# Optimization experiments

Measured on AMD Instinct MI355X. Metric: run time of the kernel, lower is better.

The kernel has to match this reference:

```python
import jax, jax.numpy as jnp
import numpy as np

B, N_PER_G, H, K, A, GNN_STEPS = 64, 100, 64, 5, 50, 3
N = B * N_PER_G  # total nodes


def _lin(key, din, dout):
    s = 1.0 / np.sqrt(din)
    kw, kb = jax.random.split(key)
    w = jax.random.uniform(kw, (din, dout), minval=-s, maxval=s, dtype=jnp.float32)
    b = jax.random.uniform(kb, (dout,), minval=-s, maxval=s, dtype=jnp.float32)
    return w, b


def setup_inputs() -> dict:
    key = jax.random.key(0)
    ks = jax.random.split(key, 16)
    # complete graph (no self loops) per batch graph
    i, j = np.meshgrid(np.arange(N_PER_G), np.arange(N_PER_G), indexing="ij")
    m = i != j
    s0, d0 = i[m], j[m]  # [n*(n-1)]
    offs = (np.arange(B) * N_PER_G)[:, None]
    src = jnp.asarray((s0[None, :] + offs).reshape(-1), dtype=jnp.int32)
    dst = jnp.asarray((d0[None, :] + offs).reshape(-1), dtype=jnp.int32)
    E = src.shape[0]
    e_type = jax.random.uniform(ks[0], (E, 2), dtype=jnp.float32)
    d = jax.random.uniform(ks[1], (E, 1), dtype=jnp.float32)
    label = jax.nn.one_hot(jax.random.randint(ks[2], (N,), 0, K), K, dtype=jnp.float32)
    actions = jax.random.randint(ks[3], (B * A, 2), 0, N_PER_G)
    l1_w, l1_b = _lin(ks[4], K, H)
    l2_w, l2_b = _lin(ks[5], H, H)
    t3_w, t3_b = _lin(ks[6], H, H)
    t4_wf, t4_b = _lin(ks[7], 1, H)
    t5_wf, t5_b = _lin(ks[8], H, 1)
    t6_w, t6_b = _lin(ks[9], H, H)
    t7_1_w, t7_1_b = _lin(ks[10], H, H)
    t7_2_w, t7_2_b = _lin(ks[11], H, H)
    t9_1_w, t9_1_b = _lin(ks[12], H, H)
    t9_2_w, t9_2_b = _lin(ks[13], H, H)
    return dict(label=label, e_type=e_type, d=d,
                l1_w=l1_w, l1_b=l1_b, l2_w=l2_w, l2_b=l2_b,
                t3_w=t3_w, t3_b=t3_b, t4_w=t4_wf[0], t4_b=t4_b,
                t5_w=t5_wf[:, 0], t5_b=t5_b, t6_w=t6_w, t6_b=t6_b,
                t7_1_w=t7_1_w, t7_1_b=t7_1_b, t7_2_w=t7_2_w, t7_2_b=t7_2_b,
                t9_1_w=t9_1_w, t9_1_b=t9_1_b, t9_2_w=t9_2_w, t9_2_b=t9_2_b,
                src=src, dst=dst, actions=actions)


def reference(label, e_type, d, l1_w, l1_b, l2_w, l2_b, t3_w, t3_b, t4_w, t4_b,
              t5_w, t5_b, t6_w, t6_b, t7_1_w, t7_1_b, t7_2_w, t7_2_b,
              t9_1_w, t9_1_b, t9_2_w, t9_2_b, src, dst, actions):
    e1 = e_type[:, 0]
    # n1_hd = h[src]*e1, n1_d = d*e1; bmm(n1_hd^T, n1_d) == sum over in-edges of h[src]*e1^2*d
    w_e = (e1 * e1) * d[:, 0]                              # [E]
    s_e = d[:, 0] * e1                                     # per-edge n1_d scalar [E]
    # sum_deg relu(t4(n1_d)) as edge-parallel relu + scatter-add
    t4_edge = jax.nn.relu(s_e[:, None] * t4_w[None, :] + t4_b)   # [E,H]
    t4_sum = jax.ops.segment_sum(t4_edge, dst, num_segments=N)   # [N,H]
    base = label @ l1_w + l1_b + t4_sum @ t3_w + t3_b            # constant across gnn steps
    h = jnp.zeros((N, H), dtype=label.dtype)
    for _ in range(GNN_STEPS):
        n1_h = jax.ops.segment_sum(h[src] * w_e[:, None], dst, num_segments=N)  # [N,H]
        h = jax.nn.relu(base + n1_h @ l2_w + l2_b)
    # readout (forward_): graph mean -> t6 stem; per-action node-pair branch
    stem = h.reshape(B, N_PER_G, H).mean(axis=1) @ t6_w + t6_b    # [B,H]
    h2 = h @ t7_1_w + t7_1_b                                      # [N,H]
    offs = jnp.repeat(jnp.arange(B, dtype=actions.dtype) * N_PER_G, A)
    a = actions + offs[:, None]                                   # global node ids [B*A,2]
    ha = h2[a[:, 0]] + h2[a[:, 1]]                                # [B*A,H]
    u = jax.nn.relu(jax.nn.relu(ha) @ t7_2_w + t7_2_b) @ t9_2_w + t9_2_b
    g_branch = jax.nn.relu(stem) @ t9_1_w + t9_1_b                # [B,H]
    q = jax.nn.relu(g_branch[:, None, :] + u.reshape(B, A, H))    # [B,A,H]
    Q_sa = q.reshape(B * A, H) @ t5_w + t5_b[0]                   # [B*A]
    return Q_sa
```

## Files before the change

kernel.cpp:

```cpp
#include <hip/hip_runtime.h>

#define HD 64
#define NPG 100
#define NGRP 64
#define NACT 50
#define EPG 9900
#define CHR 13
#define ACH 13

typedef const float* fcp;

__global__ __launch_bounds__(256)
void k_edge_base(fcp label, fcp e_type, fcp dvec,
                 fcp l1_w, fcp l1_b, fcp l2_b,
                 fcp t3_w, fcp t3_b, fcp t4_w, fcp t4_b,
                 float* __restrict__ Wt, float* __restrict__ baseo,
                 float* __restrict__ hA)
{
    const int g   = blockIdx.x >> 3;
    const int c   = blockIdx.x & 7;
    const int j0  = c * CHR;
    const int cnt = (j0 + CHR <= NPG) ? CHR : (NPG - j0);
    const int t   = threadIdx.x;
    const int hh  = t & 63;
    const int w   = t >> 6;

    __shared__ __align__(16) float s_ld[CHR * 100];
    __shared__ __align__(16) float w_ld[CHR * 100];
    __shared__ __align__(16) float t4s[CHR * HD];

    float lab[4][5], l1r[5];
    #pragma unroll
    for (int kk = 0; kk < 5; ++kk) l1r[kk] = l1_w[kk * HD + hh];
    #pragma unroll
    for (int m = 0; m < 4; ++m) {
        const int jl = w + 4 * m;
        #pragma unroll
        for (int kk = 0; kk < 5; ++kk)
            lab[m][kk] = (jl < cnt) ? label[(g * NPG + j0 + jl) * 5 + kk] : 0.f;
    }

    const float2* et2 = (const float2*)e_type;
    const int ebase = g * EPG;
    for (int idx = t; idx < CHR * 100; idx += 256) {
        const int i  = idx / CHR;
        const int jl = idx - i * CHR;
        const int j  = j0 + jl;
        if (j < NPG) {
            float s = 0.f, wv = 0.f;
            if (i != j) {
                const int e = ebase + i * 99 + j - (j > i ? 1 : 0);
                const float e1 = et2[e].x;
                const float dd = dvec[e];
                s  = dd * e1;
                wv = e1 * e1 * dd;
            }
            s_ld[jl * 100 + i] = s;
            w_ld[jl * 100 + i] = wv;
        }
    }
    __syncthreads();

    {
        float* wd = Wt + g * (NPG * NPG) + j0 * NPG;
        for (int idx = t; idx < cnt * 100; idx += 256) wd[idx] = w_ld[idx];
    }

    const float w4  = t4_w[hh];
    const float b4  = t4_b[hh];
    const float rb4 = fmaxf(b4, 0.f);
    #pragma unroll
    for (int m = 0; m < 4; ++m) {
        const int jl = w + 4 * m;
        if (jl < cnt) {
            float a0 = 0.f, a1 = 0.f, a2 = 0.f, a3 = 0.f;
            #pragma unroll 5
            for (int ib = 0; ib < 25; ++ib) {
                const float4 s4 = *(const float4*)&s_ld[jl * 100 + 4 * ib];
                a0 += fmaxf(s4.x * w4 + b4, 0.f);
                a1 += fmaxf(s4.y * w4 + b4, 0.f);
                a2 += fmaxf(s4.z * w4 + b4, 0.f);
                a3 += fmaxf(s4.w * w4 + b4, 0.f);
            }
            t4s[jl * HD + hh] = (a0 + a1) + (a2 + a3) - rb4;
        }
    }

    const float bb   = l1_b[hh] + t3_b[hh];
    const float l2bv = l2_b[hh];
    float v[4];
    #pragma unroll
    for (int m = 0; m < 4; ++m) {
        float x = bb;
        #pragma unroll
        for (int kk = 0; kk < 5; ++kk) x += lab[m][kk] * l1r[kk];
        v[m] = x;
    }
    for (int ib = 0; ib < 16; ++ib) {
        const float tw0 = t3_w[(4 * ib + 0) * HD + hh];
        const float tw1 = t3_w[(4 * ib + 1) * HD + hh];
        const float tw2 = t3_w[(4 * ib + 2) * HD + hh];
        const float tw3 = t3_w[(4 * ib + 3) * HD + hh];
        #pragma unroll
        for (int m = 0; m < 4; ++m) {
            const int jl = w + 4 * m;
            if (jl < cnt) {
                const float4 x4 = *(const float4*)&t4s[jl * HD + 4 * ib];
                v[m] += x4.x * tw0 + x4.y * tw1 + x4.z * tw2 + x4.w * tw3;
            }
        }
    }
    #pragma unroll
    for (int m = 0; m < 4; ++m) {
        const int jl = w + 4 * m;
        if (jl < cnt) {
            const int n = g * NPG + j0 + jl;
            baseo[n * HD + hh] = v[m];
            hA[n * HD + hh]    = fmaxf(v[m] + l2bv, 0.f);
        }
    }
}

__global__ __launch_bounds__(256)
void k_gnn_step(const float* __restrict__ Wt, const float* __restrict__ baseo,
                const float* __restrict__ h_old, fcp l2_w, fcp l2_b,
                float* __restrict__ h_new)
{
    const int g   = blockIdx.x >> 3;
    const int c   = blockIdx.x & 7;
    const int j0  = c * CHR;
    const int cnt = (j0 + CHR <= NPG) ? CHR : (NPG - j0);
    const int t   = threadIdx.x;
    const int hh  = t & 63;
    const int w   = t >> 6;

    __shared__ __align__(16) float hs[NPG * HD];
    __shared__ __align__(16) float wr[CHR * 100];
    __shared__ __align__(16) float n1s[CHR * HD];

    float bs[4];
    #pragma unroll
    for (int m = 0; m < 4; ++m) {
        const int jl = w + 4 * m;
        bs[m] = (jl < cnt) ? baseo[(g * NPG + j0 + jl) * HD + hh] : 0.f;
    }

    {
        const float4* ho4 = (const float4*)(h_old + g * NPG * HD);
        float4* hs4 = (float4*)hs;
        for (int idx = t; idx < NPG * HD / 4; idx += 256) hs4[idx] = ho4[idx];
        const float* wsrc = Wt + g * (NPG * NPG) + j0 * NPG;
        for (int idx = t; idx < cnt * 100; idx += 256) wr[idx] = wsrc[idx];
    }
    __syncthreads();

    float acc[4];
    #pragma unroll
    for (int m = 0; m < 4; ++m) acc[m] = 0.f;
    for (int ib = 0; ib < 25; ++ib) {
        const float h0 = hs[(4 * ib + 0) * HD + hh];
        const float h1 = hs[(4 * ib + 1) * HD + hh];
        const float h2 = hs[(4 * ib + 2) * HD + hh];
        const float h3 = hs[(4 * ib + 3) * HD + hh];
        #pragma unroll
        for (int m = 0; m < 4; ++m) {
            const int jl = w + 4 * m;
            if (jl < cnt) {
                const float4 wv = *(const float4*)&wr[jl * 100 + 4 * ib];
                acc[m] += wv.x * h0 + wv.y * h1 + wv.z * h2 + wv.w * h3;
            }
        }
    }
    #pragma unroll
    for (int m = 0; m < 4; ++m) {
        const int jl = w + 4 * m;
        if (jl < cnt) n1s[jl * HD + hh] = acc[m];
    }

    const float l2bv = l2_b[hh];
    float v[4];
    #pragma unroll
    for (int m = 0; m < 4; ++m) v[m] = bs[m] + l2bv;
    for (int ib = 0; ib < 16; ++ib) {
        const float w0 = l2_w[(4 * ib + 0) * HD + hh];
        const float w1 = l2_w[(4 * ib + 1) * HD + hh];
        const float w2 = l2_w[(4 * ib + 2) * HD + hh];
        const float w3 = l2_w[(4 * ib + 3) * HD + hh];
        #pragma unroll
        for (int m = 0; m < 4; ++m) {
            const int jl = w + 4 * m;
            if (jl < cnt) {
                const float4 x4 = *(const float4*)&n1s[jl * HD + 4 * ib];
                v[m] += x4.x * w0 + x4.y * w1 + x4.z * w2 + x4.w * w3;
            }
        }
    }
    #pragma unroll
    for (int m = 0; m < 4; ++m) {
        const int jl = w + 4 * m;
        if (jl < cnt) h_new[(g * NPG + j0 + jl) * HD + hh] = fmaxf(v[m], 0.f);
    }
}

__global__ __launch_bounds__(256)
void k_tail(const float* __restrict__ hfin, const int* __restrict__ actions,
            fcp t5_w, fcp t5_b, fcp t6_w, fcp t6_b,
            fcp t7_1_w, fcp t7_1_b, fcp t7_2_w, fcp t7_2_b,
            fcp t9_1_w, fcp t9_1_b, fcp t9_2_w, fcp t9_2_b,
            float* __restrict__ out)
{
    const int g    = blockIdx.x >> 2;
    const int c    = blockIdx.x & 3;
    const int a0g  = c * ACH;
    const int acnt = (a0g + ACH <= NACT) ? ACH : (NACT - a0g);
    const int t    = threadIdx.x;
    const int hh   = t & 63;
    const int aw   = t >> 6;

    __shared__ __align__(16) float hsb[NPG * HD];
    __shared__ __align__(16) float hsum[ACH * HD];
    __shared__ __align__(16) float r1s[ACH * HD];
    __shared__ __align__(16) float awk[4 * HD];
    __shared__ float gbuf[HD];

    int a0r[5], a1r[5];
    #pragma unroll
    for (int m = 0; m < 5; ++m) {
        const int al = aw + 3 * m;
        a0r[m] = 0; a1r[m] = 0;
        if (aw < 3 && al < acnt) {
            const int a = g * NACT + a0g + al;
            a0r[m] = actions[a * 2 + 0];
            a1r[m] = actions[a * 2 + 1];
        }
    }

    {
        const float4* hg4 = (const float4*)(hfin + g * NPG * HD);
        float4* hs4 = (float4*)hsb;
        for (int idx = t; idx < NPG * HD / 4; idx += 256) hs4[idx] = hg4[idx];
    }
    __syncthreads();

    {
        float m = 0.f;
        for (int j = aw; j < NPG; j += 4) m += hsb[j * HD + hh];
        awk[aw * HD + hh] = m;
    }
    #pragma unroll
    for (int m = 0; m < 5; ++m) {
        const int al = aw + 3 * m;
        if (aw < 3 && al < acnt)
            hsum[al * HD + hh] = hsb[a0r[m] * HD + hh] + hsb[a1r[m] * HD + hh];
    }
    __syncthreads();

    if (aw == 3) {
        float ml = (awk[0 * HD + hh] + awk[1 * HD + hh])
                 + (awk[2 * HD + hh] + awk[3 * HD + hh]);
        ml *= (1.f / NPG);
        float s = t6_b[hh];
        #pragma unroll 8
        for (int q = 0; q < HD; ++q) s += __shfl(ml, q, 64) * t6_w[q * HD + hh];
        s = fmaxf(s, 0.f);
        float gb = t9_1_b[hh];
        #pragma unroll 8
        for (int q = 0; q < HD; ++q) gb += __shfl(s, q, 64) * t9_1_w[q * HD + hh];
        gbuf[hh] = gb;
    } else {
        const float b71 = 2.f * t7_1_b[hh];
        float r[5];
        #pragma unroll
        for (int m = 0; m < 5; ++m) r[m] = b71;
        for (int ib = 0; ib < 16; ++ib) {
            const float w0 = t7_1_w[(4 * ib + 0) * HD + hh];
            const float w1 = t7_1_w[(4 * ib + 1) * HD + hh];
            const float w2 = t7_1_w[(4 * ib + 2) * HD + hh];
            const float w3 = t7_1_w[(4 * ib + 3) * HD + hh];
            #pragma unroll
            for (int m = 0; m < 5; ++m) {
                const int al = aw + 3 * m;
                if (al < acnt) {
                    const float4 x4 = *(const float4*)&hsum[al * HD + 4 * ib];
                    r[m] += x4.x * w0 + x4.y * w1 + x4.z * w2 + x4.w * w3;
                }
            }
        }
        #pragma unroll
        for (int m = 0; m < 5; ++m) {
            const int al = aw + 3 * m;
            if (al < acnt) r1s[al * HD + hh] = fmaxf(r[m], 0.f);
        }
        const float b72 = t7_2_b[hh];
        #pragma unroll
        for (int m = 0; m < 5; ++m) r[m] = b72;
        for (int ib = 0; ib < 16; ++ib) {
            const float w0 = t7_2_w[(4 * ib + 0) * HD + hh];
            const float w1 = t7_2_w[(4 * ib + 1) * HD + hh];
            const float w2 = t7_2_w[(4 * ib + 2) * HD + hh];
            const float w3 = t7_2_w[(4 * ib + 3) * HD + hh];
            #pragma unroll
            for (int m = 0; m < 5; ++m) {
                const int al = aw + 3 * m;
                if (al < acnt) {
                    const float4 x4 = *(const float4*)&r1s[al * HD + 4 * ib];
                    r[m] += x4.x * w0 + x4.y * w1 + x4.z * w2 + x4.w * w3;
                }
            }
        }
        #pragma unroll
        for (int m = 0; m < 5; ++m) {
            const int al = aw + 3 * m;
            if (al < acnt) hsum[al * HD + hh] = fmaxf(r[m], 0.f);
        }
    }
    __syncthreads();

    if (aw < 3) {
        const float b92  = t9_2_b[hh];
        const float t5wv = t5_w[hh];
        const float t5bv = t5_b[0];
        const float gbv  = gbuf[hh];
        float u[5];
        #pragma unroll
        for (int m = 0; m < 5; ++m) u[m] = b92;
        for (int ib = 0; ib < 16; ++ib) {
            const float w0 = t9_2_w[(4 * ib + 0) * HD + hh];
            const float w1 = t9_2_w[(4 * ib + 1) * HD + hh];
            const float w2 = t9_2_w[(4 * ib + 2) * HD + hh];
            const float w3 = t9_2_w[(4 * ib + 3) * HD + hh];
            #pragma unroll
            for (int m = 0; m < 5; ++m) {
                const int al = aw + 3 * m;
                if (al < acnt) {
                    const float4 x4 = *(const float4*)&hsum[al * HD + 4 * ib];
                    u[m] += x4.x * w0 + x4.y * w1 + x4.z * w2 + x4.w * w3;
                }
            }
        }
        #pragma unroll
        for (int m = 0; m < 5; ++m) {
            const int al = aw + 3 * m;
            float qv = fmaxf(gbv + u[m], 0.f) * t5wv;
            #pragma unroll
            for (int off = 32; off > 0; off >>= 1) qv += __shfl_xor(qv, off, 64);
            if (al < acnt && hh == 0) out[g * NACT + a0g + al] = qv + t5bv;
        }
    }
}

extern "C" void kernel_launch(void* const* d_in, const int* in_sizes, int n_in,
                              void* d_out, int out_size, void* d_ws, size_t ws_size,
                              hipStream_t stream)
{
    fcp label  = (fcp)d_in[0];
    fcp e_type = (fcp)d_in[1];
    fcp dvec   = (fcp)d_in[2];
    fcp l1_w   = (fcp)d_in[3];
    fcp l1_b   = (fcp)d_in[4];
    fcp l2_w   = (fcp)d_in[5];
    fcp l2_b   = (fcp)d_in[6];
    fcp t3_w   = (fcp)d_in[7];
    fcp t3_b   = (fcp)d_in[8];
    fcp t4_w   = (fcp)d_in[9];
    fcp t4_b   = (fcp)d_in[10];
    fcp t5_w   = (fcp)d_in[11];
    fcp t5_b   = (fcp)d_in[12];
    fcp t6_w   = (fcp)d_in[13];
    fcp t6_b   = (fcp)d_in[14];
    fcp t7_1_w = (fcp)d_in[15];
    fcp t7_1_b = (fcp)d_in[16];
    fcp t7_2_w = (fcp)d_in[17];
    fcp t7_2_b = (fcp)d_in[18];
    fcp t9_1_w = (fcp)d_in[19];
    fcp t9_1_b = (fcp)d_in[20];
    fcp t9_2_w = (fcp)d_in[21];
    fcp t9_2_b = (fcp)d_in[22];
    const int* actions = (const int*)d_in[25];

    char* ws = (char*)d_ws;
    float* Wt   = (float*)(ws);
    float* base = (float*)(ws + 2560000);
    float* hA   = (float*)(ws + 2560000 + 1638400);
    float* hB   = (float*)(ws + 2560000 + 2 * 1638400);

    k_edge_base<<<dim3(NGRP * 8), dim3(256), 0, stream>>>(
        label, e_type, dvec, l1_w, l1_b, l2_b, t3_w, t3_b, t4_w, t4_b,
        Wt, base, hA);
    k_gnn_step<<<dim3(NGRP * 8), dim3(256), 0, stream>>>(Wt, base, hA, l2_w, l2_b, hB);
    k_gnn_step<<<dim3(NGRP * 8), dim3(256), 0, stream>>>(Wt, base, hB, l2_w, l2_b, hA);
    k_tail<<<dim3(NGRP * 4), dim3(256), 0, stream>>>(
        hA, actions, t5_w, t5_b, t6_w, t6_b, t7_1_w, t7_1_b, t7_2_w, t7_2_b,
        t9_1_w, t9_1_b, t9_2_w, t9_2_b, (float*)d_out);
}
```

Before: 182.8 us.

## Fuse edge, GNN steps and readout into one cooperative persistent kernel

Merges the four kernels into a single cooperative launch of 256 blocks, each handling 25 target nodes of one graph, with grid.sync between GNN steps. The per-block edge weight tile and the base activations now stay in shared memory and registers, so Wt and base are no longer written to and read back from global memory. Launch overhead and inter-kernel gaps go away, at the cost of grid-wide barriers, fewer blocks (lower parallelism), h now read straight from global/L2 instead of being staged in shared memory, and more registers per thread.

```diff
diff --git a/kernel.cpp b/kernel.cpp
--- a/kernel.cpp
+++ b/kernel.cpp
@@ -1,52 +1,50 @@
 #include <hip/hip_runtime.h>
+#include <hip/hip_cooperative_groups.h>
+
+namespace cg = cooperative_groups;
 
 #define HD 64
 #define NPG 100
 #define NGRP 64
 #define NACT 50
 #define EPG 9900
-#define CHR 13
-#define ACH 13
 
 typedef const float* fcp;
 
 __global__ __launch_bounds__(256)
-void k_edge_base(fcp label, fcp e_type, fcp dvec,
-                 fcp l1_w, fcp l1_b, fcp l2_b,
-                 fcp t3_w, fcp t3_b, fcp t4_w, fcp t4_b,
-                 float* __restrict__ Wt, float* __restrict__ baseo,
-                 float* __restrict__ hA)
+void k_coop(fcp label, fcp e_type, fcp dvec,
+            fcp l1_w, fcp l1_b, fcp l2_w, fcp l2_b,
+            fcp t3_w, fcp t3_b, fcp t4_w, fcp t4_b,
+            fcp t5_w, fcp t5_b, fcp t6_w, fcp t6_b,
+            fcp t7_1_w, fcp t7_1_b, fcp t7_2_w, fcp t7_2_b,
+            fcp t9_1_w, fcp t9_1_b, fcp t9_2_w, fcp t9_2_b,
+            const int* __restrict__ actions,
+            float* __restrict__ hA, float* __restrict__ hB,
+            float* __restrict__ out)
 {
-    const int g   = blockIdx.x >> 3;
-    const int c   = blockIdx.x & 7;
-    const int j0  = c * CHR;
-    const int cnt = (j0 + CHR <= NPG) ? CHR : (NPG - j0);
-    const int t   = threadIdx.x;
-    const int hh  = t & 63;
-    const int w   = t >> 6;
-
-    __shared__ __align__(16) float s_ld[CHR * 100];
-    __shared__ __align__(16) float w_ld[CHR * 100];
-    __shared__ __align__(16) float t4s[CHR * HD];
-
-    float lab[4][5], l1r[5];
-    #pragma unroll
-    for (int kk = 0; kk < 5; ++kk) l1r[kk] = l1_w[kk * HD + hh];
-    #pragma unroll
-    for (int m = 0; m < 4; ++m) {
-        const int jl = w + 4 * m;
-        #pragma unroll
-        for (int kk = 0; kk < 5; ++kk)
-            lab[m][kk] = (jl < cnt) ? label[(g * NPG + j0 + jl) * 5 + kk] : 0.f;
-    }
-
-    const float2* et2 = (const float2*)e_type;
-    const int ebase = g * EPG;
-    for (int idx = t; idx < CHR * 100; idx += 256) {
-        const int i  = idx / CHR;
-        const int jl = idx - i * CHR;
-        const int j  = j0 + jl;
-        if (j < NPG) {
+    cg::grid_group grid = cg::this_grid();
+    const int g  = blockIdx.x >> 2;
+    const int c  = blockIdx.x & 3;
+    const int j0 = c * 25;
+    const int t  = threadIdx.x;
+    const int hh = t & 63;
+    const int w  = t >> 6;
+
+    __shared__ __align__(16) float wtc[2500];
+    __shared__ __align__(16) float buf[6400];
+    __shared__ __align__(16) float awk[4 * HD];
+    __shared__ float gbuf[HD];
+
+    float* s_ld = buf;
+    float* aux  = buf + 2500;
+
+    {
+        const float2* et2 = (const float2*)e_type;
+        const int ebase = g * EPG;
+        for (int idx = t; idx < 2500; idx += 256) {
+            const int i  = idx / 25;
+            const int jl = idx - i * 25;
+            const int j  = j0 + jl;
             float s = 0.f, wv = 0.f;
             if (i != j) {
                 const int e = ebase + i * 99 + j - (j > i ? 1 : 0);
@@ -56,23 +54,18 @@
                 wv = e1 * e1 * dd;
             }
             s_ld[jl * 100 + i] = s;
-            w_ld[jl * 100 + i] = wv;
+            wtc[jl * 100 + i] = wv;
         }
     }
     __syncthreads();
-
-    {
-        float* wd = Wt + g * (NPG * NPG) + j0 * NPG;
-        for (int idx = t; idx < cnt * 100; idx += 256) wd[idx] = w_ld[idx];
-    }
 
     const float w4  = t4_w[hh];
     const float b4  = t4_b[hh];
     const float rb4 = fmaxf(b4, 0.f);
     #pragma unroll
-    for (int m = 0; m < 4; ++m) {
+    for (int m = 0; m < 7; ++m) {
         const int jl = w + 4 * m;
-        if (jl < cnt) {
+        if (jl < 25) {
             float a0 = 0.f, a1 = 0.f, a2 = 0.f, a3 = 0.f;
             #pragma unroll 5
             for (int ib = 0; ib < 25; ++ib) {
@@ -82,180 +75,140 @@
                 a2 += fmaxf(s4.z * w4 + b4, 0.f);
                 a3 += fmaxf(s4.w * w4 + b4, 0.f);
             }
-            t4s[jl * HD + hh] = (a0 + a1) + (a2 + a3) - rb4;
-        }
-    }
-
-    const float bb   = l1_b[hh] + t3_b[hh];
+            aux[jl * HD + hh] = (a0 + a1) + (a2 + a3) - rb4;
+        }
+    }
+
+    float base_r[7];
+    {
+        float l1r[5];
+        #pragma unroll
+        for (int kk = 0; kk < 5; ++kk) l1r[kk] = l1_w[kk * HD + hh];
+        const float bb = l1_b[hh] + t3_b[hh];
+        #pragma unroll
+        for (int m = 0; m < 7; ++m) {
+            const int jl = w + 4 * m;
+            float x = bb;
+            if (jl < 25) {
+                const float* lr = &label[(g * NPG + j0 + jl) * 5];
+                #pragma unroll
+                for (int kk = 0; kk < 5; ++kk) x += lr[kk] * l1r[kk];
+            }
+            base_r[m] = x;
+        }
+        for (int ib = 0; ib < 16; ++ib) {
+            const float tw0 = t3_w[(4 * ib + 0) * HD + hh];
+            const float tw1 = t3_w[(4 * ib + 1) * HD + hh];
+            const float tw2 = t3_w[(4 * ib + 2) * HD + hh];
+            const float tw3 = t3_w[(4 * ib + 3) * HD + hh];
+            #pragma unroll
+            for (int m = 0; m < 7; ++m) {
+                const int jl = w + 4 * m;
+                if (jl < 25) {
+                    const float4 x4 = *(const float4*)&aux[jl * HD + 4 * ib];
+                    base_r[m] += x4.x * tw0 + x4.y * tw1 + x4.z * tw2 + x4.w * tw3;
+                }
+            }
+        }
+    }
     const float l2bv = l2_b[hh];
-    float v[4];
     #pragma unroll
-    for (int m = 0; m < 4; ++m) {
-        float x = bb;
-        #pragma unroll
-        for (int kk = 0; kk < 5; ++kk) x += lab[m][kk] * l1r[kk];
-        v[m] = x;
-    }
-    for (int ib = 0; ib < 16; ++ib) {
-        const float tw0 = t3_w[(4 * ib + 0) * HD + hh];
-        const float tw1 = t3_w[(4 * ib + 1) * HD + hh];
-        const float tw2 = t3_w[(4 * ib + 2) * HD + hh];
-        const float tw3 = t3_w[(4 * ib + 3) * HD + hh];
-        #pragma unroll
-        for (int m = 0; m < 4; ++m) {
+    for (int m = 0; m < 7; ++m) {
+        const int jl = w + 4 * m;
+        if (jl < 25) hA[(g * NPG + j0 + jl) * HD + hh] = fmaxf(base_r[m] + l2bv, 0.f);
+    }
+    grid.sync();
+
+    const float* hsrc = hA;
+    float*       hdst = hB;
+    for (int step = 0; step < 2; ++step) {
+        const float* hgp = hsrc + g * NPG * HD + hh;
+        float acc[7];
+        #pragma unroll
+        for (int m = 0; m < 7; ++m) acc[m] = 0.f;
+        for (int ib = 0; ib < 25; ++ib) {
+            const float h0 = hgp[(4 * ib + 0) * HD];
+            const float h1 = hgp[(4 * ib + 1) * HD];
+            const float h2 = hgp[(4 * ib + 2) * HD];
+            const float h3 = hgp[(4 * ib + 3) * HD];
+            #pragma unroll
+            for (int m = 0; m < 7; ++m) {
+                const int jl = w + 4 * m;
+                if (jl < 25) {
+                    const float4 wv = *(const float4*)&wtc[jl * 100 + 4 * ib];
+                    acc[m] += wv.x * h0 + wv.y * h1 + wv.z * h2 + wv.w * h3;
+                }
+            }
+        }
+        #pragma unroll
+        for (int m = 0; m < 7; ++m) {
             const int jl = w + 4 * m;
-            if (jl < cnt) {
-                const float4 x4 = *(const float4*)&t4s[jl * HD + 4 * ib];
-                v[m] += x4.x * tw0 + x4.y * tw1 + x4.z * tw2 + x4.w * tw3;
-            }
-        }
-    }
-    #pragma unroll
-    for (int m = 0; m < 4; ++m) {
-        const int jl = w + 4 * m;
-        if (jl < cnt) {
-            const int n = g * NPG + j0 + jl;
-            baseo[n * HD + hh] = v[m];
-            hA[n * HD + hh]    = fmaxf(v[m] + l2bv, 0.f);
-        }
-    }
-}
-
-__global__ __launch_bounds__(256)
-void k_gnn_step(const float* __restrict__ Wt, const float* __restrict__ baseo,
-                const float* __restrict__ h_old, fcp l2_w, fcp l2_b,
-                float* __restrict__ h_new)
-{
-    const int g   = blockIdx.x >> 3;
-    const int c   = blockIdx.x & 7;
-    const int j0  = c * CHR;
-    const int cnt = (j0 + CHR <= NPG) ? CHR : (NPG - j0);
-    const int t   = threadIdx.x;
-    const int hh  = t & 63;
-    const int w   = t >> 6;
-
-    __shared__ __align__(16) float hs[NPG * HD];
-    __shared__ __align__(16) float wr[CHR * 100];
-    __shared__ __align__(16) float n1s[CHR * HD];
-
-    float bs[4];
-    #pragma unroll
-    for (int m = 0; m < 4; ++m) {
-        const int jl = w + 4 * m;
-        bs[m] = (jl < cnt) ? baseo[(g * NPG + j0 + jl) * HD + hh] : 0.f;
-    }
-
-    {
-        const float4* ho4 = (const float4*)(h_old + g * NPG * HD);
-        float4* hs4 = (float4*)hs;
-        for (int idx = t; idx < NPG * HD / 4; idx += 256) hs4[idx] = ho4[idx];
-        const float* wsrc = Wt + g * (NPG * NPG) + j0 * NPG;
-        for (int idx = t; idx < cnt * 100; idx += 256) wr[idx] = wsrc[idx];
-    }
-    __syncthreads();
-
-    float acc[4];
-    #pragma unroll
-    for (int m = 0; m < 4; ++m) acc[m] = 0.f;
-    for (int ib = 0; ib < 25; ++ib) {
-        const float h0 = hs[(4 * ib + 0) * HD + hh];
-        const float h1 = hs[(4 * ib + 1) * HD + hh];
-        const float h2 = hs[(4 * ib + 2) * HD + hh];
-        const float h3 = hs[(4 * ib + 3) * HD + hh];
-        #pragma unroll
-        for (int m = 0; m < 4; ++m) {
+            if (jl < 25) aux[jl * HD + hh] = acc[m];
+        }
+        float v[7];
+        #pragma unroll
+        for (int m = 0; m < 7; ++m) v[m] = base_r[m] + l2bv;
+        for (int ib = 0; ib < 16; ++ib) {
+            const float w0 = l2_w[(4 * ib + 0) * HD + hh];
+            const float w1 = l2_w[(4 * ib + 1) * HD + hh];
+            const float w2 = l2_w[(4 * ib + 2) * HD + hh];
+            const float w3 = l2_w[(4 * ib + 3) * HD + hh];
+            #pragma unroll
+            for (int m = 0; m < 7; ++m) {
+                const int jl = w + 4 * m;
+                if (jl < 25) {
+                    const float4 x4 = *(const float4*)&aux[jl * HD + 4 * ib];
+                    v[m] += x4.x * w0 + x4.y * w1 + x4.z * w2 + x4.w * w3;
+                }
+            }
+        }
+        #pragma unroll
+        for (int m = 0; m < 7; ++m) {
             const int jl = w + 4 * m;
-            if (jl < cnt) {
-                const float4 wv = *(const float4*)&wr[jl * 100 + 4 * ib];
-                acc[m] += wv.x * h0 + wv.y * h1 + wv.z * h2 + wv.w * h3;
-            }
-        }
-    }
-    #pragma unroll
-    for (int m = 0; m < 4; ++m) {
-        const int jl = w + 4 * m;
-        if (jl < cnt) n1s[jl * HD + hh] = acc[m];
-    }
-
-    const float l2bv = l2_b[hh];
-    float v[4];
-    #pragma unroll
-    for (int m = 0; m < 4; ++m) v[m] = bs[m] + l2bv;
-    for (int ib = 0; ib < 16; ++ib) {
-        const float w0 = l2_w[(4 * ib + 0) * HD + hh];
-        const float w1 = l2_w[(4 * ib + 1) * HD + hh];
-        const float w2 = l2_w[(4 * ib + 2) * HD + hh];
-        const float w3 = l2_w[(4 * ib + 3) * HD + hh];
-        #pragma unroll
-        for (int m = 0; m < 4; ++m) {
-            const int jl = w + 4 * m;
-            if (jl < cnt) {
-                const float4 x4 = *(const float4*)&n1s[jl * HD + 4 * ib];
-                v[m] += x4.x * w0 + x4.y * w1 + x4.z * w2 + x4.w * w3;
-            }
-        }
-    }
-    #pragma unroll
-    for (int m = 0; m < 4; ++m) {
-        const int jl = w + 4 * m;
-        if (jl < cnt) h_new[(g * NPG + j0 + jl) * HD + hh] = fmaxf(v[m], 0.f);
-    }
-}
-
-__global__ __launch_bounds__(256)
-void k_tail(const float* __restrict__ hfin, const int* __restrict__ actions,
-            fcp t5_w, fcp t5_b, fcp t6_w, fcp t6_b,
-            fcp t7_1_w, fcp t7_1_b, fcp t7_2_w, fcp t7_2_b,
-            fcp t9_1_w, fcp t9_1_b, fcp t9_2_w, fcp t9_2_b,
-            float* __restrict__ out)
-{
-    const int g    = blockIdx.x >> 2;
-    const int c    = blockIdx.x & 3;
-    const int a0g  = c * ACH;
-    const int acnt = (a0g + ACH <= NACT) ? ACH : (NACT - a0g);
-    const int t    = threadIdx.x;
-    const int hh   = t & 63;
-    const int aw   = t >> 6;
-
-    __shared__ __align__(16) float hsb[NPG * HD];
-    __shared__ __align__(16) float hsum[ACH * HD];
-    __shared__ __align__(16) float r1s[ACH * HD];
-    __shared__ __align__(16) float awk[4 * HD];
-    __shared__ float gbuf[HD];
+            if (jl < 25) hdst[(g * NPG + j0 + jl) * HD + hh] = fmaxf(v[m], 0.f);
+        }
+        grid.sync();
+        const float* tmp = hsrc; hsrc = hdst; hdst = (float*)tmp;
+    }
+
+    const int a0g  = c * 13;
+    const int acnt = (c < 3) ? 13 : 11;
 
     int a0r[5], a1r[5];
     #pragma unroll
     for (int m = 0; m < 5; ++m) {
-        const int al = aw + 3 * m;
+        const int al = w + 3 * m;
         a0r[m] = 0; a1r[m] = 0;
-        if (aw < 3 && al < acnt) {
+        if (w < 3 && al < acnt) {
             const int a = g * NACT + a0g + al;
             a0r[m] = actions[a * 2 + 0];
             a1r[m] = actions[a * 2 + 1];
         }
     }
-
     {
-        const float4* hg4 = (const float4*)(hfin + g * NPG * HD);
-        float4* hs4 = (float4*)hsb;
+        const float4* hg4 = (const float4*)(hA + g * NPG * HD);
+        float4* hs4 = (float4*)buf;
         for (int idx = t; idx < NPG * HD / 4; idx += 256) hs4[idx] = hg4[idx];
     }
     __syncthreads();
+    float* hsb  = buf;
+    float* hsum = wtc;
+    float* r1s  = wtc + 832;
 
     {
-        float m = 0.f;
-        for (int j = aw; j < NPG; j += 4) m += hsb[j * HD + hh];
-        awk[aw * HD + hh] = m;
+        float mm = 0.f;
+        for (int j = w; j < NPG; j += 4) mm += hsb[j * HD + hh];
+        awk[w * HD + hh] = mm;
     }
     #pragma unroll
     for (int m = 0; m < 5; ++m) {
-        const int al = aw + 3 * m;
-        if (aw < 3 && al < acnt)
+        const int al = w + 3 * m;
+        if (w < 3 && al < acnt)
             hsum[al * HD + hh] = hsb[a0r[m] * HD + hh] + hsb[a1r[m] * HD + hh];
     }
     __syncthreads();
 
-    if (aw == 3) {
+    if (w == 3) {
         float ml = (awk[0 * HD + hh] + awk[1 * HD + hh])
                  + (awk[2 * HD + hh] + awk[3 * HD + hh]);
         ml *= (1.f / NPG);
@@ -279,7 +232,7 @@
             const float w3 = t7_1_w[(4 * ib + 3) * HD + hh];
             #pragma unroll
             for (int m = 0; m < 5; ++m) {
-                const int al = aw + 3 * m;
+                const int al = w + 3 * m;
                 if (al < acnt) {
                     const float4 x4 = *(const float4*)&hsum[al * HD + 4 * ib];
                     r[m] += x4.x * w0 + x4.y * w1 + x4.z * w2 + x4.w * w3;
@@ -288,7 +241,7 @@
         }
         #pragma unroll
         for (int m = 0; m < 5; ++m) {
-            const int al = aw + 3 * m;
+            const int al = w + 3 * m;
             if (al < acnt) r1s[al * HD + hh] = fmaxf(r[m], 0.f);
         }
         const float b72 = t7_2_b[hh];
@@ -301,7 +254,7 @@
             const float w3 = t7_2_w[(4 * ib + 3) * HD + hh];
             #pragma unroll
             for (int m = 0; m < 5; ++m) {
-                const int al = aw + 3 * m;
+                const int al = w + 3 * m;
                 if (al < acnt) {
                     const float4 x4 = *(const float4*)&r1s[al * HD + 4 * ib];
                     r[m] += x4.x * w0 + x4.y * w1 + x4.z * w2 + x4.w * w3;
@@ -310,13 +263,13 @@
         }
         #pragma unroll
         for (int m = 0; m < 5; ++m) {
-            const int al = aw + 3 * m;
+            const int al = w + 3 * m;
             if (al < acnt) hsum[al * HD + hh] = fmaxf(r[m], 0.f);
         }
     }
     __syncthreads();
 
-    if (aw < 3) {
+    if (w < 3) {
         const float b92  = t9_2_b[hh];
         const float t5wv = t5_w[hh];
         const float t5bv = t5_b[0];
@@ -331,7 +284,7 @@
             const float w3 = t9_2_w[(4 * ib + 3) * HD + hh];
             #pragma unroll
             for (int m = 0; m < 5; ++m) {
-                const int al = aw + 3 * m;
+                const int al = w + 3 * m;
                 if (al < acnt) {
                     const float4 x4 = *(const float4*)&hsum[al * HD + 4 * ib];
                     u[m] += x4.x * w0 + x4.y * w1 + x4.z * w2 + x4.w * w3;
@@ -340,7 +293,7 @@
         }
         #pragma unroll
         for (int m = 0; m < 5; ++m) {
-            const int al = aw + 3 * m;
+            const int al = w + 3 * m;
             float qv = fmaxf(gbv + u[m], 0.f) * t5wv;
             #pragma unroll
             for (int off = 32; off > 0; off >>= 1) qv += __shfl_xor(qv, off, 64);
@@ -379,17 +332,19 @@
     const int* actions = (const int*)d_in[25];
 
     char* ws = (char*)d_ws;
-    float* Wt   = (float*)(ws);
-    float* base = (float*)(ws + 2560000);
-    float* hA   = (float*)(ws + 2560000 + 1638400);
-    float* hB   = (float*)(ws + 2560000 + 2 * 1638400);
-
-    k_edge_base<<<dim3(NGRP * 8), dim3(256), 0, stream>>>(
-        label, e_type, dvec, l1_w, l1_b, l2_b, t3_w, t3_b, t4_w, t4_b,
-        Wt, base, hA);
-    k_gnn_step<<<dim3(NGRP * 8), dim3(256), 0, stream>>>(Wt, base, hA, l2_w, l2_b, hB);
-    k_gnn_step<<<dim3(NGRP * 8), dim3(256), 0, stream>>>(Wt, base, hB, l2_w, l2_b, hA);
-    k_tail<<<dim3(NGRP * 4), dim3(256), 0, stream>>>(
-        hA, actions, t5_w, t5_b, t6_w, t6_b, t7_1_w, t7_1_b, t7_2_w, t7_2_b,
-        t9_1_w, t9_1_b, t9_2_w, t9_2_b, (float*)d_out);
+    float* hA = (float*)(ws);
+    float* hB = (float*)(ws + 1638400);
+    float* outp = (float*)d_out;
+
+    void* args[] = {
+        (void*)&label, (void*)&e_type, (void*)&dvec,
+        (void*)&l1_w, (void*)&l1_b, (void*)&l2_w, (void*)&l2_b,
+        (void*)&t3_w, (void*)&t3_b, (void*)&t4_w, (void*)&t4_b,
+        (void*)&t5_w, (void*)&t5_b, (void*)&t6_w, (void*)&t6_b,
+        (void*)&t7_1_w, (void*)&t7_1_b, (void*)&t7_2_w, (void*)&t7_2_b,
+        (void*)&t9_1_w, (void*)&t9_1_b, (void*)&t9_2_w, (void*)&t9_2_b,
+        (void*)&actions, (void*)&hA, (void*)&hB, (void*)&outp
+    };
+    hipLaunchCooperativeKernel((const void*)k_coop, dim3(NGRP * 4), dim3(256),
+                               args, 0, stream);
 }
```

New measurement: 303.9 us. 66.2% more time.
